# Kernel tuning notes

Measured on AMD Instinct MI355X. Metric: run time of the kernel, lower is better.

## Reference

```python
import jax, jax.numpy as jnp
import numpy as np

N_HEAD = 16
ROPE_BASE = 10000.0


def _rotate_half(x):
    # interleaved rotate: (-x2, x1) pairs, matching torch stack+flatten
    x1 = x[..., ::2]
    x2 = x[..., 1::2]
    return jnp.stack((-x2, x1), axis=-1).reshape(x.shape)


def setup_inputs() -> dict:
    key = jax.random.key(0)
    ks = jax.random.split(key, 5)
    B, S, C = 4, 2048, 1024
    sc = 1.0 / np.sqrt(C)
    return {
        "x": jax.random.normal(ks[0], (B, S, C), jnp.float32),
        "W_qkv": jax.random.normal(ks[1], (C, 3 * C), jnp.float32) * sc,
        "b_qkv": jax.random.normal(ks[2], (3 * C,), jnp.float32) * 0.02,
        "W_proj": jax.random.normal(ks[3], (C, C), jnp.float32) * sc,
        "b_proj": jax.random.normal(ks[4], (C,), jnp.float32) * 0.02,
    }


def reference(x, W_qkv, b_qkv, W_proj, b_proj):
    B, S, C = x.shape
    H = N_HEAD
    D = C // H

    qkv = x @ W_qkv + b_qkv                       # [B,S,3C]
    q, k, v = jnp.split(qkv, 3, axis=-1)
    q = q.reshape(B, S, H, D).transpose(0, 2, 1, 3)  # [B,H,S,D]
    k = k.reshape(B, S, H, D).transpose(0, 2, 1, 3)
    v = v.reshape(B, S, H, D).transpose(0, 2, 1, 3)

    # RoPE cache (offset=0), faithful to source: emb = cat(freqs, freqs)
    inv_freq = 1.0 / (ROPE_BASE ** (jnp.arange(0, D, 2, dtype=jnp.float32) / D))
    pos = jnp.arange(S, dtype=jnp.float32)
    freqs = jnp.outer(pos, inv_freq)              # [S, D/2]
    emb = jnp.concatenate((freqs, freqs), axis=-1)  # [S, D]
    cos = jnp.cos(emb)[None, None, :, :]
    sin = jnp.sin(emb)[None, None, :, :]

    q = q * cos + _rotate_half(q) * sin
    k = k * cos + _rotate_half(k) * sin

    scale = 1.0 / jnp.sqrt(jnp.asarray(D, x.dtype))
    scores = jnp.einsum("bhqd,bhkd->bhqk", q, k) * scale  # [B,H,S,S]
    causal = jnp.tril(jnp.ones((S, S), dtype=bool))
    scores = jnp.where(causal[None, None], scores, jnp.asarray(-jnp.inf, x.dtype))
    att = jax.nn.softmax(scores, axis=-1)
    out = jnp.einsum("bhqk,bhkd->bhqd", att, v)    # [B,H,S,D]

    out = out.transpose(0, 2, 1, 3).reshape(B, S, C)
    out = out @ W_proj + b_proj                    # dropout=0 (eval)
    return out
```

## Files before the change

kernel.cpp:

```cpp
#include <hip/hip_runtime.h>
#include <hip/hip_bf16.h>
#include <math.h>

#define B_ 4
#define S_ 2048
#define C_ 1024
#define H_ 16
#define D_ 64
#define M_ (B_*S_)
#define NQKV (3*C_)
#define KDIM C_

typedef float f32x4 __attribute__((ext_vector_type(4)));
typedef float f32x16 __attribute__((ext_vector_type(16)));
typedef short bf16x8 __attribute__((ext_vector_type(8)));

static __device__ __forceinline__ ushort f2bf(float f){
    __hip_bfloat16 h = __float2bfloat16(f);
    union { __hip_bfloat16 b; ushort u; } v; v.b = h;
    return v.u;
}

static __device__ __forceinline__ void gload16(const ushort* g, ushort* l){
    __builtin_amdgcn_global_load_lds((__attribute__((address_space(1))) void*)g,
                                     (__attribute__((address_space(3))) void*)l,
                                     16, 0, 0);
}

__global__ void k_conv(const float* __restrict__ in, ushort* __restrict__ out, int n4){
    int i = blockIdx.x*blockDim.x + threadIdx.x;
    if (i < n4){
        float4 v = *(const float4*)(in + i*4);
        ushort4 o;
        o.x = f2bf(v.x); o.y = f2bf(v.y); o.z = f2bf(v.z); o.w = f2bf(v.w);
        *(ushort4*)(out + i*4) = o;
    }
}

__global__ void k_transpose(const float* __restrict__ in, ushort* __restrict__ out,
                            int R, int Ccol){
    __shared__ float tile[32][33];
    int c0 = blockIdx.x*32, r0 = blockIdx.y*32;
    int tx = threadIdx.x, ty = threadIdx.y;
    for (int j = ty; j < 32; j += 8)
        tile[j][tx] = in[(r0 + j)*Ccol + c0 + tx];
    __syncthreads();
    for (int j = ty; j < 32; j += 8)
        out[(size_t)(c0 + tx)*R + r0 + j] = f2bf(tile[j][tx]);
}

__global__ void k_cs_tab(unsigned* __restrict__ csT){
    int t = blockIdx.x*blockDim.x + threadIdx.x;
    if (t >= D_*S_) return;
    int d = t >> 11, pos = t & 2047;
    float invf = powf(10000.0f, -(float)(d & 31) / 32.0f);
    float ang = (float)pos * invf;
    csT[t] = (unsigned)f2bf(cosf(ang)) | ((unsigned)f2bf(sinf(ang)) << 16);
}

__launch_bounds__(512, 4)
__global__ void k_qkv(const ushort* __restrict__ xb, const ushort* __restrict__ wt,
                      const float* __restrict__ bqkv, const unsigned* __restrict__ csT,
                      ushort* __restrict__ qb, ushort* __restrict__ kb, ushort* __restrict__ vT){
    __shared__ __align__(16) ushort As[3][256][32];
    __shared__ __align__(16) ushort Bs[3][128][32];
    int bid = blockIdx.x;
    int lin = (bid & 7)*96 + (bid >> 3);
    int bx = lin % 24, by = lin / 24;
    int M0 = by*256, N0 = bx*128;
    int tid = threadIdx.x;
    int wid = tid >> 6, lane = tid & 63;
    int wm = wid >> 1, wn = wid & 1;
    int lrow = lane & 15, lk = lane >> 4;
    int swu = (lrow >> 1) & 3;

    int scol = (((lane & 3) ^ ((lane >> 3) & 3))) * 8;
    const ushort* gA0 = &xb[(size_t)(M0 + wid*16 + (lane >> 2))*KDIM + scol];
    const ushort* gA1 = gA0 + (size_t)128*KDIM;
    const ushort* gB0 = &wt[(size_t)(N0 + wid*16 + (lane >> 2))*KDIM + scol];

    f32x4 acc[4][4] = {};
    gload16(gA0,      &As[0][wid*16][0]);
    gload16(gA1,      &As[0][128 + wid*16][0]);
    gload16(gB0,      &Bs[0][wid*16][0]);
    gload16(gA0 + 32, &As[1][wid*16][0]);
    gload16(gA1 + 32, &As[1][128 + wid*16][0]);
    gload16(gB0 + 32, &Bs[1][wid*16][0]);

    const int NIT = KDIM/32;
    for (int i = 0; i < NIT; i++){
        if (i + 1 < NIT) asm volatile("s_waitcnt vmcnt(3) lgkmcnt(0)" ::: "memory");
        else             asm volatile("s_waitcnt vmcnt(0) lgkmcnt(0)" ::: "memory");
        __builtin_amdgcn_s_barrier();
        int pf = i + 2;
        if (pf < NIT){
            int off = pf*32;
            gload16(gA0 + off, &As[pf%3][wid*16][0]);
            gload16(gA1 + off, &As[pf%3][128 + wid*16][0]);
            gload16(gB0 + off, &Bs[pf%3][wid*16][0]);
        }
        int cur = i % 3;
        bf16x8 a[4], b[4];
#pragma unroll
        for (int mi = 0; mi < 4; mi++)
            a[mi] = *(const bf16x8*)(&As[cur][wm*64 + mi*16 + lrow][(lk ^ swu)*8]);
#pragma unroll
        for (int ni = 0; ni < 4; ni++)
            b[ni] = *(const bf16x8*)(&Bs[cur][wn*64 + ni*16 + lrow][(lk ^ swu)*8]);
#pragma unroll
        for (int mi = 0; mi < 4; mi++)
#pragma unroll
            for (int ni = 0; ni < 4; ni++)
                acc[mi][ni] = __builtin_amdgcn_mfma_f32_16x16x32_bf16(a[mi], b[ni], acc[mi][ni], 0, 0, 0);
    }
#pragma unroll
    for (int mi = 0; mi < 4; mi++)
#pragma unroll
    for (int ni = 0; ni < 4; ni++){
        int gn = N0 + wn*64 + ni*16 + lrow;
        float bias = bqkv[gn];
        int which = gn >> 10;
        int cn = gn & 1023;
        int h = cn >> 6, d = cn & 63;
        int gm0 = M0 + wm*64 + mi*16 + lk*4;
        int bb = gm0 >> 11, pos0 = gm0 & 2047;
        if (which == 2){
            ushort4 o = { f2bf(acc[mi][ni][0] + bias), f2bf(acc[mi][ni][1] + bias),
                          f2bf(acc[mi][ni][2] + bias), f2bf(acc[mi][ni][3] + bias) };
            *(ushort4*)(&vT[(((size_t)(bb*H_ + h))*D_ + d)*S_ + pos0]) = o;
        } else {
            uint4 cs4 = *(const uint4*)(&csT[d*2048 + pos0]);
            unsigned csa[4] = { cs4.x, cs4.y, cs4.z, cs4.w };
#pragma unroll
            for (int rr = 0; rr < 4; rr++){
                float val = acc[mi][ni][rr] + bias;
                float rot = __shfl_xor(val, 1);
                unsigned cs = csa[rr];
                float c = __uint_as_float(cs << 16);
                float s = __uint_as_float(cs & 0xffff0000u);
                float o = val*c + ((d & 1) ? rot : -rot)*s;
                if (which == 0) o *= 0.18033688f;
                int out_idx = (((bb*H_ + h)*S_) + pos0 + rr)*D_ + d;
                ((which == 0) ? qb : kb)[out_idx] = f2bf(o);
            }
        }
    }
}

__launch_bounds__(512, 4)
__global__ void k_proj(const ushort* __restrict__ ab, const ushort* __restrict__ wt,
                       const float* __restrict__ bias, float* __restrict__ out){
    __shared__ __align__(16) ushort As[3][256][32];
    __shared__ __align__(16) ushort Bs[3][128][32];
    int bid = blockIdx.x;
    int lin = (bid & 7)*32 + (bid >> 3);
    int bx = lin & 7, by = lin >> 3;
    int M0 = by*256, N0 = bx*128;
    int tid = threadIdx.x;
    int wid = tid >> 6, lane = tid & 63;
    int wm = wid >> 1, wn = wid & 1;
    int lrow = lane & 15, lk = lane >> 4;
    int swu = (lrow >> 1) & 3;

    int scol = (((lane & 3) ^ ((lane >> 3) & 3))) * 8;
    const ushort* gA0 = &ab[(size_t)(M0 + wid*16 + (lane >> 2))*KDIM + scol];
    const ushort* gA1 = gA0 + (size_t)128*KDIM;
    const ushort* gB0 = &wt[(size_t)(N0 + wid*16 + (lane >> 2))*KDIM + scol];

    f32x4 acc[4][4] = {};
    gload16(gA0,      &As[0][wid*16][0]);
    gload16(gA1,      &As[0][128 + wid*16][0]);
    gload16(gB0,      &Bs[0][wid*16][0]);
    gload16(gA0 + 32, &As[1][wid*16][0]);
    gload16(gA1 + 32, &As[1][128 + wid*16][0]);
    gload16(gB0 + 32, &Bs[1][wid*16][0]);

    const int NIT = KDIM/32;
    for (int i = 0; i < NIT; i++){
        if (i + 1 < NIT) asm volatile("s_waitcnt vmcnt(3) lgkmcnt(0)" ::: "memory");
        else             asm volatile("s_waitcnt vmcnt(0) lgkmcnt(0)" ::: "memory");
        __builtin_amdgcn_s_barrier();
        int pf = i + 2;
        if (pf < NIT){
            int off = pf*32;
            gload16(gA0 + off, &As[pf%3][wid*16][0]);
            gload16(gA1 + off, &As[pf%3][128 + wid*16][0]);
            gload16(gB0 + off, &Bs[pf%3][wid*16][0]);
        }
        int cur = i % 3;
        bf16x8 a[4], b[4];
#pragma unroll
        for (int mi = 0; mi < 4; mi++)
            a[mi] = *(const bf16x8*)(&As[cur][wm*64 + mi*16 + lrow][(lk ^ swu)*8]);
#pragma unroll
        for (int ni = 0; ni < 4; ni++)
            b[ni] = *(const bf16x8*)(&Bs[cur][wn*64 + ni*16 + lrow][(lk ^ swu)*8]);
#pragma unroll
        for (int mi = 0; mi < 4; mi++)
#pragma unroll
            for (int ni = 0; ni < 4; ni++)
                acc[mi][ni] = __builtin_amdgcn_mfma_f32_16x16x32_bf16(a[mi], b[ni], acc[mi][ni], 0, 0, 0);
    }
#pragma unroll
    for (int mi = 0; mi < 4; mi++)
#pragma unroll
    for (int ni = 0; ni < 4; ni++){
        int gn = N0 + wn*64 + ni*16 + lrow;
        float bv = bias[gn];
#pragma unroll
        for (int rr = 0; rr < 4; rr++){
            int gm = M0 + wm*64 + mi*16 + lk*4 + rr;
            out[(size_t)gm*C_ + gn] = acc[mi][ni][rr] + bv;
        }
    }
}

__launch_bounds__(256, 3)
__global__ void k_attn(const ushort* __restrict__ qb, const ushort* __restrict__ kb,
                       const ushort* __restrict__ vT, ushort* __restrict__ ob){
    __shared__ __align__(16) ushort Ks[64][64];
    __shared__ __align__(16) ushort Vs[64][64];
    int bh = blockIdx.x;
    int qt = (gridDim.y - 1) - blockIdx.y;
    int bb = bh >> 4, h = bh & 15;
    int tid = threadIdx.x, wid = tid >> 6, lane = tid & 63;
    int lq = lane & 31, hi = lane >> 5;
    const ushort* qp = qb + (size_t)bh*S_*D_;
    const ushort* kp = kb + (size_t)bh*S_*D_;
    const ushort* vp = vT + (size_t)bh*D_*S_;
    int qw = qt*128 + wid*32;
    int qrow = qw + lq;
    int swz = lq & 7;

    bf16x8 fq[4];
#pragma unroll
    for (int c = 0; c < 4; c++)
        fq[c] = *(const bf16x8*)(&qp[qrow*D_ + c*16 + hi*8]);

    f32x16 acc0 = {}, acc1 = {};
    float m = -1e30f, l = 0.0f;

    int tr = tid >> 3, tcu = tid & 7;
    int twu = (tcu ^ (tr & 7)) * 8;
    int tc = tcu * 8;

    int4 ra = *(const int4*)(&kp[tr*D_ + tc]);
    int4 rb = *(const int4*)(&kp[(tr+32)*D_ + tc]);
    int4 rc = *(const int4*)(&vp[(size_t)tr*S_ + tc]);
    int4 rd = *(const int4*)(&vp[(size_t)(tr+32)*S_ + tc]);

    int nit = 2*qt + 2;
    for (int it = 0; it < nit; ++it){
        int j0 = it*64;
        *(int4*)(&Ks[tr][twu])    = ra;
        *(int4*)(&Ks[tr+32][twu]) = rb;
        *(int4*)(&Vs[tr][twu])    = rc;
        *(int4*)(&Vs[tr+32][twu]) = rd;
        __syncthreads();
        if (it + 1 < nit){
            int j1 = j0 + 64;
            ra = *(const int4*)(&kp[(j1+tr)*D_ + tc]);
            rb = *(const int4*)(&kp[(j1+tr+32)*D_ + tc]);
            rc = *(const int4*)(&vp[(size_t)tr*S_ + j1 + tc]);
            rd = *(const int4*)(&vp[(size_t)(tr+32)*S_ + j1 + tc]);
        }
        int rel = qw - j0;
        if (rel >= 0){
            bool diag0 = (rel == 0);
            bool have1 = (rel >= 32);
            bool diag1 = (rel == 32);
            f32x16 z0 = {}, z1 = {};
#pragma unroll
            for (int c = 0; c < 4; c++){
                bf16x8 kf = *(const bf16x8*)(&Ks[lq][((2*c + hi) ^ swz)*8]);
                z0 = __builtin_amdgcn_mfma_f32_32x32x16_bf16(kf, fq[c], z0, 0, 0, 0);
            }
            if (have1){
#pragma unroll
                for (int c = 0; c < 4; c++){
                    bf16x8 kf = *(const bf16x8*)(&Ks[32 + lq][((2*c + hi) ^ swz)*8]);
                    z1 = __builtin_amdgcn_mfma_f32_32x32x16_bf16(kf, fq[c], z1, 0, 0, 0);
                }
            }
            if (diag0){
#pragma unroll
                for (int r = 0; r < 16; r++)
                    if (((r & 3) + 8*(r >> 2) + 4*hi) > lq) z0[r] = -1e30f;
            }
            if (diag1){
#pragma unroll
                for (int r = 0; r < 16; r++)
                    if (((r & 3) + 8*(r >> 2) + 4*hi) > lq) z1[r] = -1e30f;
            }
            float tmax = z0[0];
#pragma unroll
            for (int r = 1; r < 16; r++) tmax = fmaxf(tmax, z0[r]);
            if (have1){
#pragma unroll
                for (int r = 0; r < 16; r++) tmax = fmaxf(tmax, z1[r]);
            }
            tmax = fmaxf(tmax, __shfl_xor(tmax, 32));
            if (__any(tmax > m)){
                float newm = fmaxf(m, tmax);
                float resc = exp2f(m - newm);
                m = newm; l *= resc;
#pragma unroll
                for (int r = 0; r < 16; r++){ acc0[r] *= resc; acc1[r] *= resc; }
            }
            float rsum = 0.0f;
#pragma unroll
            for (int r = 0; r < 16; r++){ z0[r] = exp2f(z0[r] - m); rsum += z0[r]; }
            if (have1){
#pragma unroll
                for (int r = 0; r < 16; r++){ z1[r] = exp2f(z1[r] - m); rsum += z1[r]; }
            }
            rsum += __shfl_xor(rsum, 32);
            l += rsum;

#define PV_SUB(zz, r0_, su, t) do {                                              \
    unsigned w0, w1, w2, w3;                                                     \
    asm("v_cvt_pk_bf16_f32 %0, %1, %2" : "=v"(w0) : "v"(zz[r0_+0]), "v"(zz[r0_+1])); \
    asm("v_cvt_pk_bf16_f32 %0, %1, %2" : "=v"(w1) : "v"(zz[r0_+2]), "v"(zz[r0_+3])); \
    asm("v_cvt_pk_bf16_f32 %0, %1, %2" : "=v"(w2) : "v"(zz[r0_+4]), "v"(zz[r0_+5])); \
    asm("v_cvt_pk_bf16_f32 %0, %1, %2" : "=v"(w3) : "v"(zz[r0_+6]), "v"(zz[r0_+7])); \
    auto s02 = __builtin_amdgcn_permlane32_swap(w0, w2, false, false);            \
    auto s13 = __builtin_amdgcn_permlane32_swap(w1, w3, false, false);            \
    union { unsigned u[4]; bf16x8 v; } pf;                                       \
    pf.u[0] = s02[0]; pf.u[1] = s13[0]; pf.u[2] = s02[1]; pf.u[3] = s13[1];      \
    bf16x8 vf0 = *(const bf16x8*)(&Vs[lq][(((su)*4 + (t)*2 + hi) ^ swz)*8]);     \
    acc0 = __builtin_amdgcn_mfma_f32_32x32x16_bf16(vf0, pf.v, acc0, 0, 0, 0);    \
    bf16x8 vf1 = *(const bf16x8*)(&Vs[32 + lq][(((su)*4 + (t)*2 + hi) ^ swz)*8]);\
    acc1 = __builtin_amdgcn_mfma_f32_32x32x16_bf16(vf1, pf.v, acc1, 0, 0, 0);    \
} while(0)

            PV_SUB(z0, 0, 0, 0);
            PV_SUB(z0, 8, 0, 1);
            if (have1){
                PV_SUB(z1, 0, 1, 0);
                PV_SUB(z1, 8, 1, 1);
            }
#undef PV_SUB
        }
        __syncthreads();
    }
    float rl = 1.0f / l;
#pragma unroll
    for (int rg = 0; rg < 4; rg++){
        ushort4 o0 = { f2bf(acc0[rg*4+0]*rl), f2bf(acc0[rg*4+1]*rl),
                       f2bf(acc0[rg*4+2]*rl), f2bf(acc0[rg*4+3]*rl) };
        *(ushort4*)(&ob[((size_t)(bb*S_ + qrow))*C_ + h*D_ + rg*8 + hi*4]) = o0;
        ushort4 o1 = { f2bf(acc1[rg*4+0]*rl), f2bf(acc1[rg*4+1]*rl),
                       f2bf(acc1[rg*4+2]*rl), f2bf(acc1[rg*4+3]*rl) };
        *(ushort4*)(&ob[((size_t)(bb*S_ + qrow))*C_ + h*D_ + 32 + rg*8 + hi*4]) = o1;
    }
}

extern "C" void kernel_launch(void* const* d_in, const int* in_sizes, int n_in,
                              void* d_out, int out_size, void* d_ws, size_t ws_size,
                              hipStream_t stream) {
    const float* x     = (const float*)d_in[0];
    const float* Wqkv  = (const float*)d_in[1];
    const float* bqkv  = (const float*)d_in[2];
    const float* Wproj = (const float*)d_in[3];
    const float* bproj = (const float*)d_in[4];
    float* out = (float*)d_out;

    char* ws = (char*)d_ws;
    ushort*   xb   = (ushort*)(ws);
    ushort*   wqt  = (ushort*)(ws + (16u<<20));
    ushort*   wpt  = (ushort*)(ws + (22u<<20));
    unsigned* csT  = (unsigned*)(ws + (24u<<20));
    ushort*   qbuf = (ushort*)(ws + (25u<<20));
    ushort*   kbuf = (ushort*)(ws + (41u<<20));
    ushort*   vbuf = (ushort*)(ws + (57u<<20));
    ushort*   obuf = (ushort*)(ws + (73u<<20));

    k_conv<<<(M_*KDIM/4 + 255)/256, 256, 0, stream>>>(x, xb, M_*KDIM/4);
    dim3 tb(32, 8);
    k_transpose<<<dim3(NQKV/32, KDIM/32), tb, 0, stream>>>(Wqkv, wqt, KDIM, NQKV);
    k_transpose<<<dim3(C_/32, KDIM/32), tb, 0, stream>>>(Wproj, wpt, KDIM, C_);
    k_cs_tab<<<(D_*S_ + 255)/256, 256, 0, stream>>>(csT);

    k_qkv<<<768, 512, 0, stream>>>(xb, wqt, bqkv, csT, qbuf, kbuf, vbuf);
    k_attn<<<dim3(B_*H_, S_/128), 256, 0, stream>>>(qbuf, kbuf, vbuf, obuf);
    k_proj<<<256, 512, 0, stream>>>(obuf, wpt, bproj, out);
}
```

Measured before the change: 199.7 us.

## Restructure QKV and projection GEMMs to K=64 double-buffered tiles with split-phase loads

Both GEMM kernels move from a triple-buffered K=32 pipeline to double-buffered K=64 tiles. The second half of the A tile is loaded after the first half of the MFMAs, so global loads overlap with compute. The wave layout changes from 4x2 to 2x4, with an 8x2 accumulator grid per wave and a new XOR swizzle. s_setprio raises priority around the MFMA bursts. Occupancy drops from 4 to 2 blocks per CU because LDS use grows, trading latency hiding across blocks for fewer barriers per K step.

```diff
diff --git a/kernel.cpp b/kernel.cpp
--- a/kernel.cpp
+++ b/kernel.cpp
@@ -58,82 +58,108 @@
     csT[t] = (unsigned)f2bf(cosf(ang)) | ((unsigned)f2bf(sinf(ang)) << 16);
 }
 
-__launch_bounds__(512, 4)
+
+#define STAGE2(gptr, lds, b_, c0_, kt_) do {                                          \
+    gload16(gptr + (size_t)((c0_)*64)*KDIM + (kt_)*64, &lds[b_][(c0_)*64 + srow][sunit*8]);     \
+    gload16(gptr + (size_t)((c0_+1)*64)*KDIM + (kt_)*64, &lds[b_][(c0_+1)*64 + srow][sunit*8]); \
+} while(0)
+
+__launch_bounds__(512, 2)
 __global__ void k_qkv(const ushort* __restrict__ xb, const ushort* __restrict__ wt,
                       const float* __restrict__ bqkv, const unsigned* __restrict__ csT,
                       ushort* __restrict__ qb, ushort* __restrict__ kb, ushort* __restrict__ vT){
-    __shared__ __align__(16) ushort As[3][256][32];
-    __shared__ __align__(16) ushort Bs[3][128][32];
+    __shared__ __align__(16) ushort As[2][256][64];
+    __shared__ __align__(16) ushort Bs[2][128][64];
     int bid = blockIdx.x;
     int lin = (bid & 7)*96 + (bid >> 3);
     int bx = lin % 24, by = lin / 24;
     int M0 = by*256, N0 = bx*128;
     int tid = threadIdx.x;
     int wid = tid >> 6, lane = tid & 63;
-    int wm = wid >> 1, wn = wid & 1;
+    int wm = wid >> 2, wnn = wid & 3;
     int lrow = lane & 15, lk = lane >> 4;
-    int swu = (lrow >> 1) & 3;
-
-    int scol = (((lane & 3) ^ ((lane >> 3) & 3))) * 8;
-    const ushort* gA0 = &xb[(size_t)(M0 + wid*16 + (lane >> 2))*KDIM + scol];
-    const ushort* gA1 = gA0 + (size_t)128*KDIM;
-    const ushort* gB0 = &wt[(size_t)(N0 + wid*16 + (lane >> 2))*KDIM + scol];
-
-    f32x4 acc[4][4] = {};
-    gload16(gA0,      &As[0][wid*16][0]);
-    gload16(gA1,      &As[0][128 + wid*16][0]);
-    gload16(gB0,      &Bs[0][wid*16][0]);
-    gload16(gA0 + 32, &As[1][wid*16][0]);
-    gload16(gA1 + 32, &As[1][128 + wid*16][0]);
-    gload16(gB0 + 32, &Bs[1][wid*16][0]);
-
-    const int NIT = KDIM/32;
-    for (int i = 0; i < NIT; i++){
-        if (i + 1 < NIT) asm volatile("s_waitcnt vmcnt(3) lgkmcnt(0)" ::: "memory");
-        else             asm volatile("s_waitcnt vmcnt(0) lgkmcnt(0)" ::: "memory");
+    int swk = lrow & 7;
+
+    int srow = tid >> 3, sunit = tid & 7;
+    const ushort* gA = &xb[(size_t)(M0 + srow)*KDIM + (size_t)((sunit ^ (srow & 7))*8)];
+    const ushort* gB = &wt[(size_t)(N0 + srow)*KDIM + (size_t)((sunit ^ (srow & 7))*8)];
+
+    f32x4 acc[8][2] = {};
+    STAGE2(gB, Bs, 0, 0, 0);
+    STAGE2(gA, As, 0, 0, 0);
+    STAGE2(gA, As, 0, 2, 0);
+
+    const int NT = KDIM/64;
+    for (int t = 0; t < NT; t++){
+        int b = t & 1;
+        asm volatile("s_waitcnt vmcnt(2)" ::: "memory");
         __builtin_amdgcn_s_barrier();
-        int pf = i + 2;
-        if (pf < NIT){
-            int off = pf*32;
-            gload16(gA0 + off, &As[pf%3][wid*16][0]);
-            gload16(gA1 + off, &As[pf%3][128 + wid*16][0]);
-            gload16(gB0 + off, &Bs[pf%3][wid*16][0]);
-        }
-        int cur = i % 3;
-        bf16x8 a[4], b[4];
-#pragma unroll
-        for (int mi = 0; mi < 4; mi++)
-            a[mi] = *(const bf16x8*)(&As[cur][wm*64 + mi*16 + lrow][(lk ^ swu)*8]);
-#pragma unroll
-        for (int ni = 0; ni < 4; ni++)
-            b[ni] = *(const bf16x8*)(&Bs[cur][wn*64 + ni*16 + lrow][(lk ^ swu)*8]);
-#pragma unroll
-        for (int mi = 0; mi < 4; mi++)
-#pragma unroll
-            for (int ni = 0; ni < 4; ni++)
-                acc[mi][ni] = __builtin_amdgcn_mfma_f32_16x16x32_bf16(a[mi], b[ni], acc[mi][ni], 0, 0, 0);
-    }
-#pragma unroll
-    for (int mi = 0; mi < 4; mi++)
-#pragma unroll
-    for (int ni = 0; ni < 4; ni++){
-        int gn = N0 + wn*64 + ni*16 + lrow;
+        if (t + 1 < NT){
+            STAGE2(gB, Bs, b^1, 0, t+1);
+            STAGE2(gA, As, b^1, 0, t+1);
+        }
+        bf16x8 bfr[2][2], afr[4][2];
+#pragma unroll
+        for (int bn = 0; bn < 2; bn++)
+#pragma unroll
+            for (int kk = 0; kk < 2; kk++)
+                bfr[bn][kk] = *(const bf16x8*)(&Bs[b][wnn*32 + bn*16 + lrow][((kk*4 + lk) ^ swk)*8]);
+#pragma unroll
+        for (int am = 0; am < 4; am++)
+#pragma unroll
+            for (int kk = 0; kk < 2; kk++)
+                afr[am][kk] = *(const bf16x8*)(&As[b][wm*128 + am*16 + lrow][((kk*4 + lk) ^ swk)*8]);
+        __builtin_amdgcn_s_setprio(1);
+#pragma unroll
+        for (int am = 0; am < 4; am++)
+#pragma unroll
+            for (int bn = 0; bn < 2; bn++){
+                acc[am][bn] = __builtin_amdgcn_mfma_f32_16x16x32_bf16(afr[am][0], bfr[bn][0], acc[am][bn], 0, 0, 0);
+                acc[am][bn] = __builtin_amdgcn_mfma_f32_16x16x32_bf16(afr[am][1], bfr[bn][1], acc[am][bn], 0, 0, 0);
+            }
+        __builtin_amdgcn_s_setprio(0);
+        if (t + 1 < NT) asm volatile("s_waitcnt vmcnt(4)" ::: "memory");
+        else            asm volatile("s_waitcnt vmcnt(0)" ::: "memory");
+        __builtin_amdgcn_s_barrier();
+        if (t + 1 < NT) STAGE2(gA, As, b^1, 2, t+1);
+        bf16x8 afr2[4][2];
+#pragma unroll
+        for (int am = 0; am < 4; am++)
+#pragma unroll
+            for (int kk = 0; kk < 2; kk++)
+                afr2[am][kk] = *(const bf16x8*)(&As[b][wm*128 + 64 + am*16 + lrow][((kk*4 + lk) ^ swk)*8]);
+        __builtin_amdgcn_s_setprio(1);
+#pragma unroll
+        for (int am = 0; am < 4; am++)
+#pragma unroll
+            for (int bn = 0; bn < 2; bn++){
+                acc[am+4][bn] = __builtin_amdgcn_mfma_f32_16x16x32_bf16(afr2[am][0], bfr[bn][0], acc[am+4][bn], 0, 0, 0);
+                acc[am+4][bn] = __builtin_amdgcn_mfma_f32_16x16x32_bf16(afr2[am][1], bfr[bn][1], acc[am+4][bn], 0, 0, 0);
+            }
+        __builtin_amdgcn_s_setprio(0);
+    }
+#pragma unroll
+    for (int am = 0; am < 8; am++)
+#pragma unroll
+    for (int bn = 0; bn < 2; bn++){
+        int gn = N0 + wnn*32 + bn*16 + lrow;
         float bias = bqkv[gn];
         int which = gn >> 10;
         int cn = gn & 1023;
         int h = cn >> 6, d = cn & 63;
-        int gm0 = M0 + wm*64 + mi*16 + lk*4;
+        int rowoff = (am < 4) ? am*16 : 64 + (am-4)*16;
+        int gm0 = M0 + wm*128 + rowoff + lk*4;
         int bb = gm0 >> 11, pos0 = gm0 & 2047;
         if (which == 2){
-            ushort4 o = { f2bf(acc[mi][ni][0] + bias), f2bf(acc[mi][ni][1] + bias),
-                          f2bf(acc[mi][ni][2] + bias), f2bf(acc[mi][ni][3] + bias) };
+            ushort4 o = { f2bf(acc[am][bn][0] + bias), f2bf(acc[am][bn][1] + bias),
+                          f2bf(acc[am][bn][2] + bias), f2bf(acc[am][bn][3] + bias) };
             *(ushort4*)(&vT[(((size_t)(bb*H_ + h))*D_ + d)*S_ + pos0]) = o;
         } else {
             uint4 cs4 = *(const uint4*)(&csT[d*2048 + pos0]);
             unsigned csa[4] = { cs4.x, cs4.y, cs4.z, cs4.w };
 #pragma unroll
             for (int rr = 0; rr < 4; rr++){
-                float val = acc[mi][ni][rr] + bias;
+                float val = acc[am][bn][rr] + bias;
                 float rot = __shfl_xor(val, 1);
                 unsigned cs = csa[rr];
                 float c = __uint_as_float(cs << 16);
@@ -147,70 +173,90 @@
     }
 }
 
-__launch_bounds__(512, 4)
+__launch_bounds__(512, 2)
 __global__ void k_proj(const ushort* __restrict__ ab, const ushort* __restrict__ wt,
                        const float* __restrict__ bias, float* __restrict__ out){
-    __shared__ __align__(16) ushort As[3][256][32];
-    __shared__ __align__(16) ushort Bs[3][128][32];
+    __shared__ __align__(16) ushort As[2][256][64];
+    __shared__ __align__(16) ushort Bs[2][128][64];
     int bid = blockIdx.x;
     int lin = (bid & 7)*32 + (bid >> 3);
     int bx = lin & 7, by = lin >> 3;
     int M0 = by*256, N0 = bx*128;
     int tid = threadIdx.x;
     int wid = tid >> 6, lane = tid & 63;
-    int wm = wid >> 1, wn = wid & 1;
+    int wm = wid >> 2, wnn = wid & 3;
     int lrow = lane & 15, lk = lane >> 4;
-    int swu = (lrow >> 1) & 3;
-
-    int scol = (((lane & 3) ^ ((lane >> 3) & 3))) * 8;
-    const ushort* gA0 = &ab[(size_t)(M0 + wid*16 + (lane >> 2))*KDIM + scol];
-    const ushort* gA1 = gA0 + (size_t)128*KDIM;
-    const ushort* gB0 = &wt[(size_t)(N0 + wid*16 + (lane >> 2))*KDIM + scol];
-
-    f32x4 acc[4][4] = {};
-    gload16(gA0,      &As[0][wid*16][0]);
-    gload16(gA1,      &As[0][128 + wid*16][0]);
-    gload16(gB0,      &Bs[0][wid*16][0]);
-    gload16(gA0 + 32, &As[1][wid*16][0]);
-    gload16(gA1 + 32, &As[1][128 + wid*16][0]);
-    gload16(gB0 + 32, &Bs[1][wid*16][0]);
-
-    const int NIT = KDIM/32;
-    for (int i = 0; i < NIT; i++){
-        if (i + 1 < NIT) asm volatile("s_waitcnt vmcnt(3) lgkmcnt(0)" ::: "memory");
-        else             asm volatile("s_waitcnt vmcnt(0) lgkmcnt(0)" ::: "memory");
+    int swk = lrow & 7;
+
+    int srow = tid >> 3, sunit = tid & 7;
+    const ushort* gA = &ab[(size_t)(M0 + srow)*KDIM + (size_t)((sunit ^ (srow & 7))*8)];
+    const ushort* gB = &wt[(size_t)(N0 + srow)*KDIM + (size_t)((sunit ^ (srow & 7))*8)];
+
+    f32x4 acc[8][2] = {};
+    STAGE2(gB, Bs, 0, 0, 0);
+    STAGE2(gA, As, 0, 0, 0);
+    STAGE2(gA, As, 0, 2, 0);
+
+    const int NT = KDIM/64;
+    for (int t = 0; t < NT; t++){
+        int b = t & 1;
+        asm volatile("s_waitcnt vmcnt(2)" ::: "memory");
         __builtin_amdgcn_s_barrier();
-        int pf = i + 2;
-        if (pf < NIT){
-            int off = pf*32;
-            gload16(gA0 + off, &As[pf%3][wid*16][0]);
-            gload16(gA1 + off, &As[pf%3][128 + wid*16][0]);
-            gload16(gB0 + off, &Bs[pf%3][wid*16][0]);
-        }
-        int cur = i % 3;
-        bf16x8 a[4], b[4];
-#pragma unroll
-        for (int mi = 0; mi < 4; mi++)
-            a[mi] = *(const bf16x8*)(&As[cur][wm*64 + mi*16 + lrow][(lk ^ swu)*8]);
-#pragma unroll
-        for (int ni = 0; ni < 4; ni++)
-            b[ni] = *(const bf16x8*)(&Bs[cur][wn*64 + ni*16 + lrow][(lk ^ swu)*8]);
-#pragma unroll
-        for (int mi = 0; mi < 4; mi++)
-#pragma unroll
-            for (int ni = 0; ni < 4; ni++)
-                acc[mi][ni] = __builtin_amdgcn_mfma_f32_16x16x32_bf16(a[mi], b[ni], acc[mi][ni], 0, 0, 0);
-    }
-#pragma unroll
-    for (int mi = 0; mi < 4; mi++)
-#pragma unroll
-    for (int ni = 0; ni < 4; ni++){
-        int gn = N0 + wn*64 + ni*16 + lrow;
+        if (t + 1 < NT){
+            STAGE2(gB, Bs, b^1, 0, t+1);
+            STAGE2(gA, As, b^1, 0, t+1);
+        }
+        bf16x8 bfr[2][2], afr[4][2];
+#pragma unroll
+        for (int bn = 0; bn < 2; bn++)
+#pragma unroll
+            for (int kk = 0; kk < 2; kk++)
+                bfr[bn][kk] = *(const bf16x8*)(&Bs[b][wnn*32 + bn*16 + lrow][((kk*4 + lk) ^ swk)*8]);
+#pragma unroll
+        for (int am = 0; am < 4; am++)
+#pragma unroll
+            for (int kk = 0; kk < 2; kk++)
+                afr[am][kk] = *(const bf16x8*)(&As[b][wm*128 + am*16 + lrow][((kk*4 + lk) ^ swk)*8]);
+        __builtin_amdgcn_s_setprio(1);
+#pragma unroll
+        for (int am = 0; am < 4; am++)
+#pragma unroll
+            for (int bn = 0; bn < 2; bn++){
+                acc[am][bn] = __builtin_amdgcn_mfma_f32_16x16x32_bf16(afr[am][0], bfr[bn][0], acc[am][bn], 0, 0, 0);
+                acc[am][bn] = __builtin_amdgcn_mfma_f32_16x16x32_bf16(afr[am][1], bfr[bn][1], acc[am][bn], 0, 0, 0);
+            }
+        __builtin_amdgcn_s_setprio(0);
+        if (t + 1 < NT) asm volatile("s_waitcnt vmcnt(4)" ::: "memory");
+        else            asm volatile("s_waitcnt vmcnt(0)" ::: "memory");
+        __builtin_amdgcn_s_barrier();
+        if (t + 1 < NT) STAGE2(gA, As, b^1, 2, t+1);
+        bf16x8 afr2[4][2];
+#pragma unroll
+        for (int am = 0; am < 4; am++)
+#pragma unroll
+            for (int kk = 0; kk < 2; kk++)
+                afr2[am][kk] = *(const bf16x8*)(&As[b][wm*128 + 64 + am*16 + lrow][((kk*4 + lk) ^ swk)*8]);
+        __builtin_amdgcn_s_setprio(1);
+#pragma unroll
+        for (int am = 0; am < 4; am++)
+#pragma unroll
+            for (int bn = 0; bn < 2; bn++){
+                acc[am+4][bn] = __builtin_amdgcn_mfma_f32_16x16x32_bf16(afr2[am][0], bfr[bn][0], acc[am+4][bn], 0, 0, 0);
+                acc[am+4][bn] = __builtin_amdgcn_mfma_f32_16x16x32_bf16(afr2[am][1], bfr[bn][1], acc[am+4][bn], 0, 0, 0);
+            }
+        __builtin_amdgcn_s_setprio(0);
+    }
+#pragma unroll
+    for (int am = 0; am < 8; am++)
+#pragma unroll
+    for (int bn = 0; bn < 2; bn++){
+        int gn = N0 + wnn*32 + bn*16 + lrow;
         float bv = bias[gn];
+        int rowoff = (am < 4) ? am*16 : 64 + (am-4)*16;
 #pragma unroll
         for (int rr = 0; rr < 4; rr++){
-            int gm = M0 + wm*64 + mi*16 + lk*4 + rr;
-            out[(size_t)gm*C_ + gn] = acc[mi][ni][rr] + bv;
+            int gm = M0 + wm*128 + rowoff + lk*4 + rr;
+            out[(size_t)gm*C_ + gn] = acc[am][bn][rr] + bv;
         }
     }
 }
```

New measurement: 224.7 us. 1.13x slower.
